# Kernel tuning notes

Measured on AMD Instinct MI355X. Metric: run time of the kernel, lower is better.

## Reference

```python
import jax, jax.numpy as jnp
import numpy as np

NEG_INF_CONST = -2.0**32 + 1.0  # matches torch module's self.inf


def setup_inputs() -> dict:
    key = jax.random.key(0)
    kq, kk, kv = jax.random.split(key, 3)
    B, L, S, H, E, D = 2, 2048, 2048, 8, 64, 64
    return {
        "queries": jax.random.normal(kq, (B, L, H, E), dtype=jnp.float32),
        "keys": jax.random.normal(kk, (B, S, H, E), dtype=jnp.float32),
        "values": jax.random.normal(kv, (B, S, H, D), dtype=jnp.float32),
    }


def reference(queries, keys, values):
    B, L, H, E = queries.shape
    _, S, _, D = values.shape
    scale = 1.0 / np.sqrt(E).astype(np.float32)
    # Faithful to torch: .view(B*H, L, E) on a contiguous [B, L, H, E] tensor
    # reinterprets memory row-major (mixes L and H), same as jnp.reshape.
    q = queries.reshape(B * H, L, E)
    k = keys.reshape(B * H, S, E)
    # squared pairwise L2 distance == cdist(...).pow(2)
    d2 = (
        jnp.sum(q * q, axis=-1)[:, :, None]
        + jnp.sum(k * k, axis=-1)[:, None, :]
        - 2.0 * jnp.einsum("nle,nse->nls", q, k)
    )
    d2 = jnp.maximum(d2, 0.0).reshape(B, H, L, S)
    scores = 1.0 - jnp.exp(-d2)  # dropout is identity in eval mode
    causal = jnp.tril(jnp.ones((L, S), dtype=bool))  # mask.tril(diagonal=0)
    scores = jnp.where(causal, scores, jnp.float32(NEG_INF_CONST))
    A = jax.nn.softmax(scale * scores, axis=-1)
    return jnp.einsum("bhls,bshd->blhd", A, values)
```

## Files before the change

kernel.cpp:

```cpp
#include <hip/hip_runtime.h>
#include <hip/hip_bf16.h>

typedef __attribute__((ext_vector_type(8))) __bf16 bf16x8;
typedef __attribute__((ext_vector_type(4))) float f32x4;

namespace {

constexpr int L = 2048;
constexpr int E = 64;
constexpr int NHEAD = 16;
constexpr float SCALE = 0.125f;
constexpr float LOG2E = 1.44269504f;
constexpr float TWO_LOG2E = 2.88539008f;

constexpr size_t KN_OFF = 4096;
constexpr size_t KB_OFF = KN_OFF + (size_t)NHEAD * L * 4;
constexpr size_t VT_OFF = KB_OFF + (size_t)NHEAD * L * E * 2;

__device__ __forceinline__ int swz(int row, int byte_in_row) {
  const int f = (row & 3) | (((row >> 3) & 1) << 2);
  return row * 128 + (byte_in_row ^ (f << 4));
}

__device__ __forceinline__ unsigned pack_bf16(float a, float b) {
  union { __bf16 h[2]; unsigned u; } p;
  p.h[0] = (__bf16)a; p.h[1] = (__bf16)b;
  return p.u;
}

__device__ __forceinline__ void cvt_row16(const float4* src, float& pn,
                                          bf16x8& w0, bf16x8& w1) {
  float4 a = src[0], c = src[1];
  pn += a.x*a.x + a.y*a.y + a.z*a.z + a.w*a.w;
  pn += c.x*c.x + c.y*c.y + c.z*c.z + c.w*c.w;
  w0[0]=(__bf16)a.x; w0[1]=(__bf16)a.y; w0[2]=(__bf16)a.z; w0[3]=(__bf16)a.w;
  w0[4]=(__bf16)c.x; w0[5]=(__bf16)c.y; w0[6]=(__bf16)c.z; w0[7]=(__bf16)c.w;
  float4 d = src[2], e = src[3];
  pn += d.x*d.x + d.y*d.y + d.z*d.z + d.w*d.w;
  pn += e.x*e.x + e.y*e.y + e.z*e.z + e.w*e.w;
  w1[0]=(__bf16)d.x; w1[1]=(__bf16)d.y; w1[2]=(__bf16)d.z; w1[3]=(__bf16)d.w;
  w1[4]=(__bf16)e.x; w1[5]=(__bf16)e.y; w1[6]=(__bf16)e.z; w1[7]=(__bf16)e.w;
}

__global__ __launch_bounds__(256)
void prep(const float* __restrict__ Kg, const float* __restrict__ Vg,
          __bf16* __restrict__ Kb, float* __restrict__ kn,
          __bf16* __restrict__ Vt) {
  __shared__ float Vs[64][65];
  const int t = threadIdx.x;
  if (blockIdx.x < 512) {
    const int row = blockIdx.x * 64 + (t >> 2);
    const int seg = t & 3;
    const float4* src = reinterpret_cast<const float4*>(
        Kg + (size_t)row * E + seg * 16);
    float pn = 0.f; bf16x8 w0, w1;
    cvt_row16(src, pn, w0, w1);
    __bf16* dst = Kb + (size_t)row * E + seg * 16;
    *reinterpret_cast<bf16x8*>(dst)     = w0;
    *reinterpret_cast<bf16x8*>(dst + 8) = w1;
    pn += __shfl_xor(pn, 1);
    pn += __shfl_xor(pn, 2);
    if (seg == 0) kn[row] = -LOG2E * pn;
  } else {
    const int bb = blockIdx.x - 512;
    const int n  = bb >> 5;
    const int st = bb & 31;
    const int b = n >> 3, h = n & 7;
    {
      const int srow = t >> 2, seg = t & 3;
      const float4* src = reinterpret_cast<const float4*>(
          Vg + ((size_t)b * L + st * 64 + srow) * 512 + h * 64 + seg * 16);
      #pragma unroll
      for (int j = 0; j < 4; ++j) {
        float4 a = src[j];
        Vs[srow][seg*16 + j*4 + 0] = a.x;
        Vs[srow][seg*16 + j*4 + 1] = a.y;
        Vs[srow][seg*16 + j*4 + 2] = a.z;
        Vs[srow][seg*16 + j*4 + 3] = a.w;
      }
    }
    __syncthreads();
    {
      const int d = t >> 2, sg = t & 3;
      bf16x8 o0, o1;
      #pragma unroll
      for (int i = 0; i < 8; ++i) o0[i] = (__bf16)Vs[sg*16 + i][d];
      #pragma unroll
      for (int i = 0; i < 8; ++i) o1[i] = (__bf16)Vs[sg*16 + 8 + i][d];
      __bf16* dst = Vt + (size_t)n * (E * L) + (size_t)d * L + st * 64 + sg * 16;
      *reinterpret_cast<bf16x8*>(dst)     = o0;
      *reinterpret_cast<bf16x8*>(dst + 8) = o1;
    }
  }
}

__global__ __launch_bounds__(512, 4)
void degr_attn(const float* __restrict__ Qg, const __bf16* __restrict__ Kb,
               const __bf16* __restrict__ Vt, const float* __restrict__ kng,
               float* __restrict__ Og) {
  __shared__ char smem[65536];

  const int id = blockIdx.x;
  const int n  = (id & 7) | (((id >> 3) & 1) << 3);
  const int u  = id >> 4;
  const int lt = 31 - u;
  const int l0 = lt * 64;
  const int b = n >> 3, h = n & 7;

  const int t = threadIdx.x;
  const int wave = t >> 6, grp = wave >> 2, w4 = wave & 3;
  const int lane = t & 63, lg = lane >> 4, lr = lane & 15;
  const int gt = t & 255;

  char* kbase = smem + grp * 32768;
  char* vbase = smem + grp * 32768 + 16384;
  float*  Cbuf = (float*)smem;
  float*  Dbuf = (float*)(smem + 17408);

  const float*  Qh  = Qg  + (size_t)n * (L * E);
  const __bf16* Kh  = Kb  + (size_t)n * (L * E);
  const __bf16* Vh  = Vt  + (size_t)n * (E * L);
  const float*  knh = kng + (size_t)n * L;

  const int l_glob = l0 + 16 * w4 + lr;
  bf16x8 qf0, qf1;
  float qnL;
  {
    const float* qp = Qh + (size_t)l_glob * E + 8 * lg;
    float4 a = *reinterpret_cast<const float4*>(qp);
    float4 d = *reinterpret_cast<const float4*>(qp + 4);
    float4 a2 = *reinterpret_cast<const float4*>(qp + 32);
    float4 d2v = *reinterpret_cast<const float4*>(qp + 36);
    float pn = 0.f;
    #pragma unroll
    for (int i = 0; i < 4; ++i) {
      float v0 = (i==0)?a.x:(i==1)?a.y:(i==2)?a.z:a.w;
      float v1 = (i==0)?d.x:(i==1)?d.y:(i==2)?d.z:d.w;
      float v2 = (i==0)?a2.x:(i==1)?a2.y:(i==2)?a2.z:a2.w;
      float v3 = (i==0)?d2v.x:(i==1)?d2v.y:(i==2)?d2v.z:d2v.w;
      qf0[i]   = (__bf16)v0;  qf0[i+4] = (__bf16)v1;
      qf1[i]   = (__bf16)v2;  qf1[i+4] = (__bf16)v3;
      float f;
      f = (float)qf0[i];   pn += f*f;
      f = (float)qf0[i+4]; pn += f*f;
      f = (float)qf1[i];   pn += f*f;
      f = (float)qf1[i+4]; pn += f*f;
    }
    pn += __shfl_xor(pn, 16);
    pn += __shfl_xor(pn, 32);
    qnL = -LOG2E * pn;
  }

  const int srow = gt >> 2;
  const int scol = (gt & 3) * 2;
  const int wk0 = swz(srow, scol*16);
  const int wk1 = swz(srow, scol*16 + 16);
  int koffL[4], koffH[4];
  #pragma unroll
  for (int hx = 0; hx < 4; ++hx) {
    const int krow = 32*(hx>>1) + 8*(lr>>2) + 4*(hx&1) + (lr&3);
    koffL[hx] = swz(krow, lg*16);
    koffH[hx] = swz(krow, 64 + lg*16);
  }
  int voff[2][4];
  #pragma unroll
  for (int sc = 0; sc < 2; ++sc)
    #pragma unroll
    for (int dsb = 0; dsb < 4; ++dsb)
      voff[sc][dsb] = swz(dsb*16 + lr, sc*64 + lg*16);

  bf16x8 kr0, kr1, vr0, vr1;
  auto loadKV = [&](int c) {
    const int s0 = c * 64;
    const __bf16* kp = Kh + (size_t)(s0 + srow) * E + scol * 8;
    kr0 = *reinterpret_cast<const bf16x8*>(kp);
    kr1 = *reinterpret_cast<const bf16x8*>(kp + 8);
    const __bf16* vp = Vh + (size_t)srow * L + s0 + scol * 8;
    vr0 = *reinterpret_cast<const bf16x8*>(vp);
    vr1 = *reinterpret_cast<const bf16x8*>(vp + 8);
  };
  auto writeKV = [&](int WB) {
    *reinterpret_cast<bf16x8*>(kbase + WB + wk0) = kr0;
    *reinterpret_cast<bf16x8*>(kbase + WB + wk1) = kr1;
    *reinterpret_cast<bf16x8*>(vbase + WB + wk0) = vr0;
    *reinterpret_cast<bf16x8*>(vbase + WB + wk1) = vr1;
  };

  const int n_it = (lt >> 1) + 1;
  loadKV(grp <= lt ? grp : lt);
  writeKV(0);
  __syncthreads();

  f32x4 oacc[4];
  #pragma unroll
  for (int i = 0; i < 4; ++i) oacc[i] = (f32x4){0.f, 0.f, 0.f, 0.f};
  float den = 0.f;

  auto body = [&](int i, const int B, const bool MASK) {
    const int c = 2 * i + grp;
    const bool more = (i + 1 < n_it);
    if (more) {
      int cn = 2 * (i + 1) + grp;
      loadKV(cn <= lt ? cn : lt);
    }
    const int s_base = c * 64;
    const char* kb = kbase + B;
    const char* vb = vbase + B;

    float4 kn4[4];
    kn4[0] = *reinterpret_cast<const float4*>(knh + s_base + 8*lg);
    kn4[1] = *reinterpret_cast<const float4*>(knh + s_base + 8*lg + 4);
    kn4[2] = *reinterpret_cast<const float4*>(knh + s_base + 32 + 8*lg);
    kn4[3] = *reinterpret_cast<const float4*>(knh + s_base + 36 + 8*lg);

    __builtin_amdgcn_s_setprio(1);
    unsigned up[4][2];
    #pragma unroll
    for (int hx = 0; hx < 4; ++hx) {
      const bf16x8 kf0 = *reinterpret_cast<const bf16x8*>(kb + koffL[hx]);
      const bf16x8 kf1 = *reinterpret_cast<const bf16x8*>(kb + koffH[hx]);
      f32x4 acc = (f32x4){0.f, 0.f, 0.f, 0.f};
      acc = __builtin_amdgcn_mfma_f32_16x16x32_bf16(kf0, qf0, acc, 0, 0, 0);
      acc = __builtin_amdgcn_mfma_f32_16x16x32_bf16(kf1, qf1, acc, 0, 0, 0);
      float w[4];
      #pragma unroll
      for (int r = 0; r < 4; ++r) {
        const float knv = (r==0)?kn4[hx].x:(r==1)?kn4[hx].y:(r==2)?kn4[hx].z:kn4[hx].w;
        float arg = fminf(fmaf(TWO_LOG2E, acc[r], qnL + knv), 0.f);
        float e1  = exp2f(arg);
        float y   = fmaf(-SCALE, e1, SCALE);
        float tt  = fmaf(0.5f, y, 1.0f);
        float wv  = fmaf(y, tt, 1.0f);
        if (MASK) {
          const int sof = 32*(hx>>1) + 8*lg + 4*(hx&1);
          wv = (s_base + sof + r <= l_glob) ? wv : 0.f;
        }
        den += wv;
        w[r] = wv;
      }
      up[hx][0] = pack_bf16(w[0], w[1]);
      up[hx][1] = pack_bf16(w[2], w[3]);
    }
    #pragma unroll
    for (int sc = 0; sc < 2; ++sc) {
      union { unsigned u[4]; bf16x8 v; } pb;
      pb.u[0] = up[2*sc][0];
      pb.u[1] = up[2*sc][1];
      pb.u[2] = up[2*sc+1][0];
      pb.u[3] = up[2*sc+1][1];
      const bf16x8 pf = pb.v;
      #pragma unroll
      for (int dsb = 0; dsb < 4; ++dsb) {
        const bf16x8 vf = *reinterpret_cast<const bf16x8*>(vb + voff[sc][dsb]);
        oacc[dsb] = __builtin_amdgcn_mfma_f32_16x16x32_bf16(pf, vf, oacc[dsb], 0, 0, 0);
      }
    }
    __builtin_amdgcn_s_setprio(0);

    if (more) writeKV(B ^ 8192);
    __syncthreads();
  };

  {
    int i = 0;
    for (; i + 2 < n_it; i += 2) { body(i, 0, false); body(i + 1, 8192, false); }
    if ((n_it & 1) == 0) { body(n_it - 2, 0, false); body(n_it - 1, 8192, true); }
    else                 { body(n_it - 1, 0, true); }
  }

  den += __shfl_xor(den, 16);
  den += __shfl_xor(den, 32);

  if (grp == 1) {
    #pragma unroll
    for (int dsb = 0; dsb < 4; ++dsb)
      #pragma unroll
      for (int r = 0; r < 4; ++r)
        Cbuf[(16*w4 + 4*lg + r) * 65 + 16*dsb + lr] = oacc[dsb][r];
    if (lane < 16) Dbuf[16*w4 + lr] = den;
  }
  __syncthreads();
  if (grp == 0) {
    const float dtot = den + Dbuf[16*w4 + lr];
    float inv[4];
    #pragma unroll
    for (int r = 0; r < 4; ++r)
      inv[r] = 1.0f / __shfl(dtot, 4*lg + r);
    float* obase = Og + ((size_t)b * L + l0 + 16*w4) * 512 + h * 64;
    #pragma unroll
    for (int r = 0; r < 4; ++r) {
      float* orow = obase + (size_t)(4*lg + r) * 512;
      #pragma unroll
      for (int dsb = 0; dsb < 4; ++dsb) {
        const float s = oacc[dsb][r] + Cbuf[(16*w4 + 4*lg + r) * 65 + 16*dsb + lr];
        orow[16*dsb + lr] = s * inv[r];
      }
    }
  }
}

}

extern "C" void kernel_launch(void* const* d_in, const int* in_sizes, int n_in,
                              void* d_out, int out_size, void* d_ws, size_t ws_size,
                              hipStream_t stream) {
  (void)in_sizes; (void)n_in; (void)out_size; (void)ws_size;
  const float* q = (const float*)d_in[0];
  const float* k = (const float*)d_in[1];
  const float* v = (const float*)d_in[2];
  float*       o = (float*)d_out;

  char* ws = (char*)d_ws;
  float*  kn = (float*)(ws + KN_OFF);
  __bf16* Kb = (__bf16*)(ws + KB_OFF);
  __bf16* Vt = (__bf16*)(ws + VT_OFF);

  prep<<<dim3(1024), dim3(256), 0, stream>>>(k, v, Kb, kn, Vt);
  degr_attn<<<dim3(512), dim3(512), 0, stream>>>(q, Kb, Vt, kn, o);
}
```

Before: 44.00 us.

## Split each query tile's KV range across four wave groups with 1024-thread blocks

Block size doubles to 1024 threads, and the causal KV range for each 64-row query tile is now split across four wave groups instead of two. Each group walks every fourth KV chunk. The per-group K/V staging drops from double-buffered to single-buffered, so each iteration needs an extra barrier between compute and the shared-memory write. At the end, three groups spill their partial outputs and denominators to LDS and group 0 sums them before normalising. The aim is to shorten the serial per-block loop and add parallelism per query tile, at the cost of less load/compute overlap, more barriers and a larger final reduction.

Measured after the change: 118.5 us. 2.69x slower.

```diff
diff --git a/kernel.cpp b/kernel.cpp
--- a/kernel.cpp
+++ b/kernel.cpp
@@ -94,7 +94,7 @@
   }
 }
 
-__global__ __launch_bounds__(512, 4)
+__global__ __launch_bounds__(1024, 8)
 void degr_attn(const float* __restrict__ Qg, const __bf16* __restrict__ Kb,
                const __bf16* __restrict__ Vt, const float* __restrict__ kng,
                float* __restrict__ Og) {
@@ -112,10 +112,8 @@
   const int lane = t & 63, lg = lane >> 4, lr = lane & 15;
   const int gt = t & 255;
 
-  char* kbase = smem + grp * 32768;
-  char* vbase = smem + grp * 32768 + 16384;
-  float*  Cbuf = (float*)smem;
-  float*  Dbuf = (float*)(smem + 17408);
+  char* kbase = smem + grp * 16384;
+  char* vbase = kbase + 8192;
 
   const float*  Qh  = Qg  + (size_t)n * (L * E);
   const __bf16* Kh  = Kb  + (size_t)n * (L * E);
@@ -179,34 +177,20 @@
     vr0 = *reinterpret_cast<const bf16x8*>(vp);
     vr1 = *reinterpret_cast<const bf16x8*>(vp + 8);
   };
-  auto writeKV = [&](int WB) {
-    *reinterpret_cast<bf16x8*>(kbase + WB + wk0) = kr0;
-    *reinterpret_cast<bf16x8*>(kbase + WB + wk1) = kr1;
-    *reinterpret_cast<bf16x8*>(vbase + WB + wk0) = vr0;
-    *reinterpret_cast<bf16x8*>(vbase + WB + wk1) = vr1;
+  auto writeKV = [&]() {
+    *reinterpret_cast<bf16x8*>(kbase + wk0) = kr0;
+    *reinterpret_cast<bf16x8*>(kbase + wk1) = kr1;
+    *reinterpret_cast<bf16x8*>(vbase + wk0) = vr0;
+    *reinterpret_cast<bf16x8*>(vbase + wk1) = vr1;
   };
-
-  const int n_it = (lt >> 1) + 1;
-  loadKV(grp <= lt ? grp : lt);
-  writeKV(0);
-  __syncthreads();
 
   f32x4 oacc[4];
   #pragma unroll
   for (int i = 0; i < 4; ++i) oacc[i] = (f32x4){0.f, 0.f, 0.f, 0.f};
   float den = 0.f;
 
-  auto body = [&](int i, const int B, const bool MASK) {
-    const int c = 2 * i + grp;
-    const bool more = (i + 1 < n_it);
-    if (more) {
-      int cn = 2 * (i + 1) + grp;
-      loadKV(cn <= lt ? cn : lt);
-    }
+  auto compute = [&](int c, bool MASK) {
     const int s_base = c * 64;
-    const char* kb = kbase + B;
-    const char* vb = vbase + B;
-
     float4 kn4[4];
     kn4[0] = *reinterpret_cast<const float4*>(knh + s_base + 8*lg);
     kn4[1] = *reinterpret_cast<const float4*>(knh + s_base + 8*lg + 4);
@@ -217,8 +201,8 @@
     unsigned up[4][2];
     #pragma unroll
     for (int hx = 0; hx < 4; ++hx) {
-      const bf16x8 kf0 = *reinterpret_cast<const bf16x8*>(kb + koffL[hx]);
-      const bf16x8 kf1 = *reinterpret_cast<const bf16x8*>(kb + koffH[hx]);
+      const bf16x8 kf0 = *reinterpret_cast<const bf16x8*>(kbase + koffL[hx]);
+      const bf16x8 kf1 = *reinterpret_cast<const bf16x8*>(kbase + koffH[hx]);
       f32x4 acc = (f32x4){0.f, 0.f, 0.f, 0.f};
       acc = __builtin_amdgcn_mfma_f32_16x16x32_bf16(kf0, qf0, acc, 0, 0, 0);
       acc = __builtin_amdgcn_mfma_f32_16x16x32_bf16(kf1, qf1, acc, 0, 0, 0);
@@ -251,37 +235,54 @@
       const bf16x8 pf = pb.v;
       #pragma unroll
       for (int dsb = 0; dsb < 4; ++dsb) {
-        const bf16x8 vf = *reinterpret_cast<const bf16x8*>(vb + voff[sc][dsb]);
+        const bf16x8 vf = *reinterpret_cast<const bf16x8*>(vbase + voff[sc][dsb]);
         oacc[dsb] = __builtin_amdgcn_mfma_f32_16x16x32_bf16(pf, vf, oacc[dsb], 0, 0, 0);
       }
     }
     __builtin_amdgcn_s_setprio(0);
-
-    if (more) writeKV(B ^ 8192);
+  };
+
+  const int n_it = (lt >> 2) + 1;
+  loadKV(grp <= lt ? grp : lt);
+  writeKV();
+  __syncthreads();
+
+  int i = 0;
+  for (; i < n_it - 1; ++i) {
+    const int cn = 4 * (i + 1) + grp;
+    loadKV(cn <= lt ? cn : lt);
+    compute(4 * i + grp, false);
     __syncthreads();
-  };
-
+    writeKV();
+    __syncthreads();
+  }
   {
-    int i = 0;
-    for (; i + 2 < n_it; i += 2) { body(i, 0, false); body(i + 1, 8192, false); }
-    if ((n_it & 1) == 0) { body(n_it - 2, 0, false); body(n_it - 1, 8192, true); }
-    else                 { body(n_it - 1, 0, true); }
+    const int c = 4 * i + grp;
+    if (c <= lt) compute(c, true);
+    __syncthreads();
   }
 
   den += __shfl_xor(den, 16);
   den += __shfl_xor(den, 32);
 
-  if (grp == 1) {
+  float* Cb0 = (float*)smem;
+  float* Cb1 = (float*)(smem + 16640);
+  float* Cb2 = (float*)(smem + 33280);
+  float* Db  = (float*)(smem + 49920);
+
+  if (grp > 0) {
+    float* C = (float*)(smem + (grp - 1) * 16640);
     #pragma unroll
     for (int dsb = 0; dsb < 4; ++dsb)
       #pragma unroll
       for (int r = 0; r < 4; ++r)
-        Cbuf[(16*w4 + 4*lg + r) * 65 + 16*dsb + lr] = oacc[dsb][r];
-    if (lane < 16) Dbuf[16*w4 + lr] = den;
+        C[(16*w4 + 4*lg + r) * 65 + 16*dsb + lr] = oacc[dsb][r];
+    if (lane < 16) Db[(grp - 1) * 64 + 16*w4 + lr] = den;
   }
   __syncthreads();
   if (grp == 0) {
-    const float dtot = den + Dbuf[16*w4 + lr];
+    const int row16 = 16*w4 + lr;
+    const float dtot = den + Db[row16] + Db[64 + row16] + Db[128 + row16];
     float inv[4];
     #pragma unroll
     for (int r = 0; r < 4; ++r)
@@ -290,9 +291,11 @@
     #pragma unroll
     for (int r = 0; r < 4; ++r) {
       float* orow = obase + (size_t)(4*lg + r) * 512;
+      const int ci = (16*w4 + 4*lg + r) * 65 + lr;
       #pragma unroll
       for (int dsb = 0; dsb < 4; ++dsb) {
-        const float s = oacc[dsb][r] + Cbuf[(16*w4 + 4*lg + r) * 65 + 16*dsb + lr];
+        const float s = oacc[dsb][r]
+                      + Cb0[ci + 16*dsb] + Cb1[ci + 16*dsb] + Cb2[ci + 16*dsb];
         orow[16*dsb + lr] = s * inv[r];
       }
     }
@@ -316,5 +319,5 @@
   __bf16* Vt = (__bf16*)(ws + VT_OFF);
 
   prep<<<dim3(1024), dim3(256), 0, stream>>>(k, v, Kb, kn, Vt);
-  degr_attn<<<dim3(512), dim3(512), 0, stream>>>(q, Kb, Vt, kn, o);
-}
+  degr_attn<<<dim3(512), dim3(1024), 0, stream>>>(q, Kb, Vt, kn, o);
+}
```

## Split KV range four ways across blocks with a separate merge kernel

Applied to the files above, without the earlier changes.

Moves the attention kernel to a split-K scheme. Each 256-thread block handles one query tile and one of four interleaved key-chunk subsets, writes unnormalized partial outputs and denominators to workspace, and a new merge kernel sums the four partials and normalizes. V fragments are now read straight from global memory rather than staged through LDS, and shared memory shrinks to a single K buffer. The aim is more parallelism and occupancy, at the cost of an extra kernel launch, partial-result traffic through global memory, and the loss of K/V double buffering.

Measured after the change: 123.1 us. 180% more time.

```diff
diff --git a/kernel.cpp b/kernel.cpp
--- a/kernel.cpp
+++ b/kernel.cpp
@@ -16,6 +16,8 @@
 constexpr size_t KN_OFF = 4096;
 constexpr size_t KB_OFF = KN_OFF + (size_t)NHEAD * L * 4;
 constexpr size_t VT_OFF = KB_OFF + (size_t)NHEAD * L * E * 2;
+constexpr size_t P_OFF  = VT_OFF + (size_t)NHEAD * E * L * 2;
+constexpr size_t D_OFF  = P_OFF + (size_t)4 * NHEAD * L * E * 4;
 
 __device__ __forceinline__ int swz(int row, int byte_in_row) {
   const int f = (row & 3) | (((row >> 3) & 1) << 2);
@@ -71,12 +73,12 @@
       const float4* src = reinterpret_cast<const float4*>(
           Vg + ((size_t)b * L + st * 64 + srow) * 512 + h * 64 + seg * 16);
       #pragma unroll
-      for (int j = 0; j < 4; ++j) {
-        float4 a = src[j];
-        Vs[srow][seg*16 + j*4 + 0] = a.x;
-        Vs[srow][seg*16 + j*4 + 1] = a.y;
-        Vs[srow][seg*16 + j*4 + 2] = a.z;
-        Vs[srow][seg*16 + j*4 + 3] = a.w;
+      for (int jj = 0; jj < 4; ++jj) {
+        float4 a = src[jj];
+        Vs[srow][seg*16 + jj*4 + 0] = a.x;
+        Vs[srow][seg*16 + jj*4 + 1] = a.y;
+        Vs[srow][seg*16 + jj*4 + 2] = a.z;
+        Vs[srow][seg*16 + jj*4 + 3] = a.w;
       }
     }
     __syncthreads();
@@ -94,209 +96,194 @@
   }
 }
 
-__global__ __launch_bounds__(512, 4)
+__global__ __launch_bounds__(256, 8)
 void degr_attn(const float* __restrict__ Qg, const __bf16* __restrict__ Kb,
                const __bf16* __restrict__ Vt, const float* __restrict__ kng,
-               float* __restrict__ Og) {
-  __shared__ char smem[65536];
+               float* __restrict__ Pp, float* __restrict__ Dp) {
+  __shared__ char smem[8192];
 
   const int id = blockIdx.x;
-  const int n  = (id & 7) | (((id >> 3) & 1) << 3);
-  const int u  = id >> 4;
-  const int lt = 31 - u;
+  const int n  = id & 15;
+  const int v  = id >> 4;
+  const int w  = v & 15, k = v >> 4;
+  const int lt = (k < 4) ? w : (31 - w);
+  const int j  = k & 3;
   const int l0 = lt * 64;
-  const int b = n >> 3, h = n & 7;
 
   const int t = threadIdx.x;
-  const int wave = t >> 6, grp = wave >> 2, w4 = wave & 3;
+  const int w4 = t >> 6;
   const int lane = t & 63, lg = lane >> 4, lr = lane & 15;
-  const int gt = t & 255;
-
-  char* kbase = smem + grp * 32768;
-  char* vbase = smem + grp * 32768 + 16384;
-  float*  Cbuf = (float*)smem;
-  float*  Dbuf = (float*)(smem + 17408);
-
-  const float*  Qh  = Qg  + (size_t)n * (L * E);
-  const __bf16* Kh  = Kb  + (size_t)n * (L * E);
-  const __bf16* Vh  = Vt  + (size_t)n * (E * L);
-  const float*  knh = kng + (size_t)n * L;
-
-  const int l_glob = l0 + 16 * w4 + lr;
-  bf16x8 qf0, qf1;
-  float qnL;
-  {
-    const float* qp = Qh + (size_t)l_glob * E + 8 * lg;
-    float4 a = *reinterpret_cast<const float4*>(qp);
-    float4 d = *reinterpret_cast<const float4*>(qp + 4);
-    float4 a2 = *reinterpret_cast<const float4*>(qp + 32);
-    float4 d2v = *reinterpret_cast<const float4*>(qp + 36);
-    float pn = 0.f;
-    #pragma unroll
-    for (int i = 0; i < 4; ++i) {
-      float v0 = (i==0)?a.x:(i==1)?a.y:(i==2)?a.z:a.w;
-      float v1 = (i==0)?d.x:(i==1)?d.y:(i==2)?d.z:d.w;
-      float v2 = (i==0)?a2.x:(i==1)?a2.y:(i==2)?a2.z:a2.w;
-      float v3 = (i==0)?d2v.x:(i==1)?d2v.y:(i==2)?d2v.z:d2v.w;
-      qf0[i]   = (__bf16)v0;  qf0[i+4] = (__bf16)v1;
-      qf1[i]   = (__bf16)v2;  qf1[i+4] = (__bf16)v3;
-      float f;
-      f = (float)qf0[i];   pn += f*f;
-      f = (float)qf0[i+4]; pn += f*f;
-      f = (float)qf1[i];   pn += f*f;
-      f = (float)qf1[i+4]; pn += f*f;
-    }
-    pn += __shfl_xor(pn, 16);
-    pn += __shfl_xor(pn, 32);
-    qnL = -LOG2E * pn;
-  }
-
-  const int srow = gt >> 2;
-  const int scol = (gt & 3) * 2;
-  const int wk0 = swz(srow, scol*16);
-  const int wk1 = swz(srow, scol*16 + 16);
-  int koffL[4], koffH[4];
-  #pragma unroll
-  for (int hx = 0; hx < 4; ++hx) {
-    const int krow = 32*(hx>>1) + 8*(lr>>2) + 4*(hx&1) + (lr&3);
-    koffL[hx] = swz(krow, lg*16);
-    koffH[hx] = swz(krow, 64 + lg*16);
-  }
-  int voff[2][4];
-  #pragma unroll
-  for (int sc = 0; sc < 2; ++sc)
-    #pragma unroll
-    for (int dsb = 0; dsb < 4; ++dsb)
-      voff[sc][dsb] = swz(dsb*16 + lr, sc*64 + lg*16);
-
-  bf16x8 kr0, kr1, vr0, vr1;
-  auto loadKV = [&](int c) {
-    const int s0 = c * 64;
-    const __bf16* kp = Kh + (size_t)(s0 + srow) * E + scol * 8;
-    kr0 = *reinterpret_cast<const bf16x8*>(kp);
-    kr1 = *reinterpret_cast<const bf16x8*>(kp + 8);
-    const __bf16* vp = Vh + (size_t)srow * L + s0 + scol * 8;
-    vr0 = *reinterpret_cast<const bf16x8*>(vp);
-    vr1 = *reinterpret_cast<const bf16x8*>(vp + 8);
-  };
-  auto writeKV = [&](int WB) {
-    *reinterpret_cast<bf16x8*>(kbase + WB + wk0) = kr0;
-    *reinterpret_cast<bf16x8*>(kbase + WB + wk1) = kr1;
-    *reinterpret_cast<bf16x8*>(vbase + WB + wk0) = vr0;
-    *reinterpret_cast<bf16x8*>(vbase + WB + wk1) = vr1;
-  };
-
-  const int n_it = (lt >> 1) + 1;
-  loadKV(grp <= lt ? grp : lt);
-  writeKV(0);
-  __syncthreads();
 
   f32x4 oacc[4];
   #pragma unroll
   for (int i = 0; i < 4; ++i) oacc[i] = (f32x4){0.f, 0.f, 0.f, 0.f};
   float den = 0.f;
 
-  auto body = [&](int i, const int B, const bool MASK) {
-    const int c = 2 * i + grp;
-    const bool more = (i + 1 < n_it);
-    if (more) {
-      int cn = 2 * (i + 1) + grp;
-      loadKV(cn <= lt ? cn : lt);
-    }
-    const int s_base = c * 64;
-    const char* kb = kbase + B;
-    const char* vb = vbase + B;
-
-    float4 kn4[4];
-    kn4[0] = *reinterpret_cast<const float4*>(knh + s_base + 8*lg);
-    kn4[1] = *reinterpret_cast<const float4*>(knh + s_base + 8*lg + 4);
-    kn4[2] = *reinterpret_cast<const float4*>(knh + s_base + 32 + 8*lg);
-    kn4[3] = *reinterpret_cast<const float4*>(knh + s_base + 36 + 8*lg);
-
-    __builtin_amdgcn_s_setprio(1);
-    unsigned up[4][2];
+  const int l_glob = l0 + 16 * w4 + lr;
+
+  if (j <= lt) {
+    const float*  Qh  = Qg  + (size_t)n * (L * E);
+    const __bf16* Kh  = Kb  + (size_t)n * (L * E);
+    const __bf16* Vh  = Vt  + (size_t)n * (E * L);
+    const float*  knh = kng + (size_t)n * L;
+
+    bf16x8 qf0, qf1;
+    float qnL;
+    {
+      const float* qp = Qh + (size_t)l_glob * E + 8 * lg;
+      float4 a = *reinterpret_cast<const float4*>(qp);
+      float4 d = *reinterpret_cast<const float4*>(qp + 4);
+      float4 a2 = *reinterpret_cast<const float4*>(qp + 32);
+      float4 d2v = *reinterpret_cast<const float4*>(qp + 36);
+      float pn = 0.f;
+      #pragma unroll
+      for (int i = 0; i < 4; ++i) {
+        float v0 = (i==0)?a.x:(i==1)?a.y:(i==2)?a.z:a.w;
+        float v1 = (i==0)?d.x:(i==1)?d.y:(i==2)?d.z:d.w;
+        float v2 = (i==0)?a2.x:(i==1)?a2.y:(i==2)?a2.z:a2.w;
+        float v3 = (i==0)?d2v.x:(i==1)?d2v.y:(i==2)?d2v.z:d2v.w;
+        qf0[i]   = (__bf16)v0;  qf0[i+4] = (__bf16)v1;
+        qf1[i]   = (__bf16)v2;  qf1[i+4] = (__bf16)v3;
+        float f;
+        f = (float)qf0[i];   pn += f*f;
+        f = (float)qf0[i+4]; pn += f*f;
+        f = (float)qf1[i];   pn += f*f;
+        f = (float)qf1[i+4]; pn += f*f;
+      }
+      pn += __shfl_xor(pn, 16);
+      pn += __shfl_xor(pn, 32);
+      qnL = -LOG2E * pn;
+    }
+
+    const int srow = t >> 2;
+    const int scol = (t & 3) * 2;
+    const int wk0 = swz(srow, scol*16);
+    const int wk1 = swz(srow, scol*16 + 16);
+    int koffL[4], koffH[4];
     #pragma unroll
     for (int hx = 0; hx < 4; ++hx) {
-      const bf16x8 kf0 = *reinterpret_cast<const bf16x8*>(kb + koffL[hx]);
-      const bf16x8 kf1 = *reinterpret_cast<const bf16x8*>(kb + koffH[hx]);
-      f32x4 acc = (f32x4){0.f, 0.f, 0.f, 0.f};
-      acc = __builtin_amdgcn_mfma_f32_16x16x32_bf16(kf0, qf0, acc, 0, 0, 0);
-      acc = __builtin_amdgcn_mfma_f32_16x16x32_bf16(kf1, qf1, acc, 0, 0, 0);
-      float w[4];
-      #pragma unroll
-      for (int r = 0; r < 4; ++r) {
-        const float knv = (r==0)?kn4[hx].x:(r==1)?kn4[hx].y:(r==2)?kn4[hx].z:kn4[hx].w;
-        float arg = fminf(fmaf(TWO_LOG2E, acc[r], qnL + knv), 0.f);
-        float e1  = exp2f(arg);
-        float y   = fmaf(-SCALE, e1, SCALE);
-        float tt  = fmaf(0.5f, y, 1.0f);
-        float wv  = fmaf(y, tt, 1.0f);
-        if (MASK) {
-          const int sof = 32*(hx>>1) + 8*lg + 4*(hx&1);
-          wv = (s_base + sof + r <= l_glob) ? wv : 0.f;
+      const int krow = 32*(hx>>1) + 8*(lr>>2) + 4*(hx&1) + (lr&3);
+      koffL[hx] = swz(krow, lg*16);
+      koffH[hx] = swz(krow, 64 + lg*16);
+    }
+
+    bf16x8 kr0, kr1;
+    auto loadK = [&](int c) {
+      const __bf16* kp = Kh + (size_t)(c * 64 + srow) * E + scol * 8;
+      kr0 = *reinterpret_cast<const bf16x8*>(kp);
+      kr1 = *reinterpret_cast<const bf16x8*>(kp + 8);
+    };
+    auto writeK = [&]() {
+      *reinterpret_cast<bf16x8*>(smem + wk0) = kr0;
+      *reinterpret_cast<bf16x8*>(smem + wk1) = kr1;
+    };
+
+    auto compute = [&](int c, bool MASK) {
+      const int s_base = c * 64;
+      float4 kn4[4];
+      kn4[0] = *reinterpret_cast<const float4*>(knh + s_base + 8*lg);
+      kn4[1] = *reinterpret_cast<const float4*>(knh + s_base + 8*lg + 4);
+      kn4[2] = *reinterpret_cast<const float4*>(knh + s_base + 32 + 8*lg);
+      kn4[3] = *reinterpret_cast<const float4*>(knh + s_base + 36 + 8*lg);
+
+      __builtin_amdgcn_s_setprio(1);
+      unsigned up[4][2];
+      #pragma unroll
+      for (int hx = 0; hx < 4; ++hx) {
+        const bf16x8 kf0 = *reinterpret_cast<const bf16x8*>(smem + koffL[hx]);
+        const bf16x8 kf1 = *reinterpret_cast<const bf16x8*>(smem + koffH[hx]);
+        f32x4 acc = (f32x4){0.f, 0.f, 0.f, 0.f};
+        acc = __builtin_amdgcn_mfma_f32_16x16x32_bf16(kf0, qf0, acc, 0, 0, 0);
+        acc = __builtin_amdgcn_mfma_f32_16x16x32_bf16(kf1, qf1, acc, 0, 0, 0);
+        float wv4[4];
+        #pragma unroll
+        for (int r = 0; r < 4; ++r) {
+          const float knv = (r==0)?kn4[hx].x:(r==1)?kn4[hx].y:(r==2)?kn4[hx].z:kn4[hx].w;
+          float arg = fminf(fmaf(TWO_LOG2E, acc[r], qnL + knv), 0.f);
+          float e1  = exp2f(arg);
+          float y   = fmaf(-SCALE, e1, SCALE);
+          float tt  = fmaf(0.5f, y, 1.0f);
+          float wv  = fmaf(y, tt, 1.0f);
+          if (MASK) {
+            const int sof = 32*(hx>>1) + 8*lg + 4*(hx&1);
+            wv = (s_base + sof + r <= l_glob) ? wv : 0.f;
+          }
+          den += wv;
+          wv4[r] = wv;
         }
-        den += wv;
-        w[r] = wv;
-      }
-      up[hx][0] = pack_bf16(w[0], w[1]);
-      up[hx][1] = pack_bf16(w[2], w[3]);
-    }
-    #pragma unroll
-    for (int sc = 0; sc < 2; ++sc) {
-      union { unsigned u[4]; bf16x8 v; } pb;
-      pb.u[0] = up[2*sc][0];
-      pb.u[1] = up[2*sc][1];
-      pb.u[2] = up[2*sc+1][0];
-      pb.u[3] = up[2*sc+1][1];
-      const bf16x8 pf = pb.v;
-      #pragma unroll
-      for (int dsb = 0; dsb < 4; ++dsb) {
-        const bf16x8 vf = *reinterpret_cast<const bf16x8*>(vb + voff[sc][dsb]);
-        oacc[dsb] = __builtin_amdgcn_mfma_f32_16x16x32_bf16(pf, vf, oacc[dsb], 0, 0, 0);
-      }
-    }
-    __builtin_amdgcn_s_setprio(0);
-
-    if (more) writeKV(B ^ 8192);
+        up[hx][0] = pack_bf16(wv4[0], wv4[1]);
+        up[hx][1] = pack_bf16(wv4[2], wv4[3]);
+      }
+      #pragma unroll
+      for (int sc = 0; sc < 2; ++sc) {
+        union { unsigned u[4]; bf16x8 vv; } pb;
+        pb.u[0] = up[2*sc][0];
+        pb.u[1] = up[2*sc][1];
+        pb.u[2] = up[2*sc+1][0];
+        pb.u[3] = up[2*sc+1][1];
+        const bf16x8 pf = pb.vv;
+        #pragma unroll
+        for (int dsb = 0; dsb < 4; ++dsb) {
+          const __bf16* vp = Vh + (size_t)(dsb*16 + lr) * L + s_base + sc*32 + lg*8;
+          const bf16x8 vf = *reinterpret_cast<const bf16x8*>(vp);
+          oacc[dsb] = __builtin_amdgcn_mfma_f32_16x16x32_bf16(pf, vf, oacc[dsb], 0, 0, 0);
+        }
+      }
+      __builtin_amdgcn_s_setprio(0);
+    };
+
+    const int n_it = ((lt - j) >> 2) + 1;
+    loadK(j);
+    writeK();
     __syncthreads();
-  };
-
-  {
-    int i = 0;
-    for (; i + 2 < n_it; i += 2) { body(i, 0, false); body(i + 1, 8192, false); }
-    if ((n_it & 1) == 0) { body(n_it - 2, 0, false); body(n_it - 1, 8192, true); }
-    else                 { body(n_it - 1, 0, true); }
+    for (int i = 0; i < n_it; ++i) {
+      const int c = 4 * i + j;
+      const bool more = (i + 1 < n_it);
+      if (more) loadK(c + 4);
+      compute(c, c == lt);
+      if (more) {
+        __syncthreads();
+        writeK();
+        __syncthreads();
+      }
+    }
   }
 
   den += __shfl_xor(den, 16);
   den += __shfl_xor(den, 32);
 
-  if (grp == 1) {
-    #pragma unroll
-    for (int dsb = 0; dsb < 4; ++dsb)
-      #pragma unroll
-      for (int r = 0; r < 4; ++r)
-        Cbuf[(16*w4 + 4*lg + r) * 65 + 16*dsb + lr] = oacc[dsb][r];
-    if (lane < 16) Dbuf[16*w4 + lr] = den;
-  }
-  __syncthreads();
-  if (grp == 0) {
-    const float dtot = den + Dbuf[16*w4 + lr];
-    float inv[4];
-    #pragma unroll
-    for (int r = 0; r < 4; ++r)
-      inv[r] = 1.0f / __shfl(dtot, 4*lg + r);
-    float* obase = Og + ((size_t)b * L + l0 + 16*w4) * 512 + h * 64;
+  {
+    float* pb = Pp + ((size_t)(j * 16 + n) * L + (l0 + 16 * w4)) * 64;
     #pragma unroll
     for (int r = 0; r < 4; ++r) {
-      float* orow = obase + (size_t)(4*lg + r) * 512;
-      #pragma unroll
-      for (int dsb = 0; dsb < 4; ++dsb) {
-        const float s = oacc[dsb][r] + Cbuf[(16*w4 + 4*lg + r) * 65 + 16*dsb + lr];
-        orow[16*dsb + lr] = s * inv[r];
-      }
-    }
+      float* prow = pb + (size_t)(4*lg + r) * 64;
+      #pragma unroll
+      for (int dsb = 0; dsb < 4; ++dsb)
+        prow[dsb*16 + lr] = oacc[dsb][r];
+    }
+    if (lane < 16)
+      Dp[(size_t)(j * 16 + n) * L + l0 + 16 * w4 + lr] = den;
   }
+}
+
+__global__ __launch_bounds__(256)
+void merge(const float* __restrict__ Pp, const float* __restrict__ Dp,
+           float* __restrict__ Og) {
+  const int gid = blockIdx.x * 256 + threadIdx.x;
+  const int nq = gid >> 4, d4 = gid & 15;
+  const int n = nq >> 11, q = nq & 2047;
+  const float4* P4 = reinterpret_cast<const float4*>(Pp);
+  float sx = 0.f, sy = 0.f, sz = 0.f, sw = 0.f, den = 0.f;
+  #pragma unroll
+  for (int jj = 0; jj < 4; ++jj) {
+    const float4 p = P4[((size_t)(jj << 15) + nq) * 16 + d4];
+    sx += p.x; sy += p.y; sz += p.z; sw += p.w;
+    den += Dp[(size_t)(jj << 15) + nq];
+  }
+  const float inv = 1.0f / den;
+  float4 o; o.x = sx * inv; o.y = sy * inv; o.z = sz * inv; o.w = sw * inv;
+  float* op = Og + ((size_t)(n >> 3) * L + q) * 512 + (n & 7) * 64 + d4 * 4;
+  *reinterpret_cast<float4*>(op) = o;
 }
 
 }
@@ -314,7 +301,10 @@
   float*  kn = (float*)(ws + KN_OFF);
   __bf16* Kb = (__bf16*)(ws + KB_OFF);
   __bf16* Vt = (__bf16*)(ws + VT_OFF);
+  float*  Pp = (float*)(ws + P_OFF);
+  float*  Dp = (float*)(ws + D_OFF);
 
   prep<<<dim3(1024), dim3(256), 0, stream>>>(k, v, Kb, kn, Vt);
-  degr_attn<<<dim3(512), dim3(512), 0, stream>>>(q, Kb, Vt, kn, o);
-}
+  degr_attn<<<dim3(2048), dim3(256), 0, stream>>>(q, Kb, Vt, kn, Pp, Dp);
+  merge<<<dim3(2048), dim3(256), 0, stream>>>(Pp, Dp, o);
+}
```
